# Performance work log

Hardware: AMD Instinct MI355X
Metric: run time of the kernel (lower is better)

The kernel has to match this reference:

```python
import jax, jax.numpy as jnp
import numpy as np


def setup_inputs() -> dict:
    key = jax.random.key(0)
    k1, k2, k3 = jax.random.split(key, 3)
    B, C, H, W = 4, 256, 96, 128
    F = 9
    return {
        "input1": jax.random.normal(k1, (B, C, H, W), dtype=jnp.float32),
        "input2": jax.random.normal(k2, (B, C, H, W), dtype=jnp.float32),
        "weights": jax.random.normal(k3, (C, F, F), dtype=jnp.float32),
        "filter_size": 9,
        "dilation": 2,
        "num_groups": 4,
    }


def _weighted_corr(input1, input2, weights, filter_size, dilation, num_groups):
    B, C, H, W = input1.shape
    F = filter_size
    G = num_groups
    Cg = C // G
    r = F // 2
    pad = r * dilation
    # zero-pad input2 spatially so out-of-bounds displacements contribute 0
    p2 = jnp.pad(input2, ((0, 0), (0, 0), (pad, pad), (pad, pad)))
    in1g = input1.reshape(B, G, Cg, H, W)
    outs = []  # one [B, G, H, W] map per window offset (dy, dx)
    for dy in range(F):
        for dx in range(F):
            shifted = p2[:, :, dy * dilation:dy * dilation + H,
                         dx * dilation:dx * dilation + W].reshape(B, G, Cg, H, W)
            wg = weights[:, dy, dx].reshape(G, Cg)
            outs.append(jnp.einsum('bgchw,bgchw,gc->bghw', in1g, shifted, wg))
    out = jnp.stack(outs, axis=2)  # [B, G, F*F, H, W]
    return out.reshape(B, G * F * F, H, W)


def reference(input1, input2, weights, filter_size, dilation, num_groups):
    return _weighted_corr(input1, input2, weights, filter_size, dilation, num_groups)
```

## Files before the change

### kernel.cpp

```cpp
#include <hip/hip_runtime.h>

#define B_   4
#define C_   256
#define H_   96
#define W_   128
#define F_   9
#define G_   4
#define CG   64
#define NC4  16
#define NO   81
#define TH   2
#define TCOLS (W_ + 16)
#define HW_  (H_ * W_)

#define NDY   3
#define PROWS (2 * NDY)
#define PTE   (PROWS * TCOLS)
#define PNK   4

typedef _Float16 half2v __attribute__((ext_vector_type(2)));
typedef unsigned u32x2 __attribute__((ext_vector_type(2)));

__device__ __forceinline__ half2v u2h(unsigned u) {
    half2v h; __builtin_memcpy(&h, &u, 4); return h;
}
__device__ __forceinline__ half2v pkrtz(float a, float b) {
    auto r = __builtin_amdgcn_cvt_pkrtz(a, b);
    half2v h; __builtin_memcpy(&h, &r, 4); return h;
}
__device__ __forceinline__ unsigned pkrtz_u(float a, float b) {
    auto r = __builtin_amdgcn_cvt_pkrtz(a, b);
    unsigned u; __builtin_memcpy(&u, &r, 4); return u;
}

#if __has_builtin(__builtin_amdgcn_fdot2)
#define FDOT2(a, b, c) __builtin_amdgcn_fdot2((a), (b), (c), false)
#else
__device__ __forceinline__ float fdot2_fb(half2v a, half2v b, float c) {
    return c + (float)a[0] * (float)b[0] + (float)a[1] * (float)b[1];
}
#define FDOT2(a, b, c) fdot2_fb((a), (b), (c))
#endif

__global__ void pack_weights_kernel(const float* __restrict__ w,
                                    u32x2* __restrict__ wp) {
    int i = blockIdx.x * blockDim.x + threadIdx.x;
    if (i >= G_ * NC4 * NO) return;
    int o  = i % NO;
    int c4 = (i / NO) % NC4;
    int g  = i / (NO * NC4);
    const float* base = w + (size_t)(g * CG + 4 * c4) * NO + o;
    u32x2 r;
    r.x = pkrtz_u(base[0], base[NO]);
    r.y = pkrtz_u(base[2 * NO], base[3 * NO]);
    wp[i] = r;
}

template <bool PACKED>
__global__ __launch_bounds__(256)
void wcorr_kernel(const float* __restrict__ in1, const float* __restrict__ in2,
                  const u32x2* __restrict__ wp, const float* __restrict__ wraw,
                  float* __restrict__ out) {
    __shared__ u32x2 tile[2][PTE];

    int bid  = blockIdx.x;
    int xcd  = bid & 7;
    int slot = bid >> 3;
    int pair = xcd + 8 * (slot / 144);
    int rem  = slot % 144;
    int pass = rem / 48;
    int hblk = rem % 48;
    int b = pair >> 2, g = pair & 3;
    int h0 = hblk * TH;

    int t  = threadIdx.x;
    int ty = t >> 7;
    int tx = t & 127;

    const float* in1g = in1 + (size_t)(b * C_ + g * CG) * HW_;
    const float* in2g = in2 + (size_t)(b * C_ + g * CG) * HW_;

    const int gr0 = h0 - 8 + 6 * pass;
    int po[PNK];
#pragma unroll
    for (int k = 0; k < PNK; ++k) {
        int idx = k * 256 + t;
        int row = idx / TCOLS;
        int col = idx - row * TCOLS;
        int gr  = gr0 + row;
        int gc  = col - 8;
        bool inb = (idx < PTE) && (gr >= 0) && (gr < H_) && (gc >= 0) && (gc < W_);
        po[k] = inb ? (gr * W_ + gc) : -1;
    }

    float acc[NDY * F_];
#pragma unroll
    for (int o = 0; o < NDY * F_; ++o) acc[o] = 0.f;

#pragma unroll
    for (int k = 0; k < PNK; ++k) {
        int idx = k * 256 + t;
        float v0 = 0.f, v1 = 0.f, v2 = 0.f, v3 = 0.f;
        if (po[k] >= 0) {
            const float* p = in2g + po[k];
            v0 = p[0]; v1 = p[HW_]; v2 = p[2 * HW_]; v3 = p[3 * HW_];
        }
        if (idx < PTE) {
            u32x2 r; r.x = pkrtz_u(v0, v1); r.y = pkrtz_u(v2, v3);
            tile[0][idx] = r;
        }
    }

    const int in1off = (h0 + ty) * W_ + tx;
    float a0 = in1g[in1off], a1 = in1g[in1off + HW_];
    float a2 = in1g[in1off + 2 * HW_], a3 = in1g[in1off + 3 * HW_];

    const int lbase = ty * TCOLS + tx;

    for (int c4 = 0; c4 < NC4; ++c4) {
        const bool more = (c4 + 1 < NC4);

        float v0[PNK], v1[PNK], v2[PNK], v3[PNK];
        if (more) {
            const float* chb = in2g + (size_t)(4 * (c4 + 1)) * HW_;
#pragma unroll
            for (int k = 0; k < PNK; ++k) {
                v0[k] = 0.f; v1[k] = 0.f; v2[k] = 0.f; v3[k] = 0.f;
                if (po[k] >= 0) {
                    const float* p = chb + po[k];
                    v0[k] = p[0]; v1[k] = p[HW_];
                    v2[k] = p[2 * HW_]; v3[k] = p[3 * HW_];
                }
            }
        }

        __syncthreads();

        if (more) {
            u32x2* dst = tile[(c4 + 1) & 1];
#pragma unroll
            for (int k = 0; k < PNK; ++k) {
                int idx = k * 256 + t;
                if (idx < PTE) {
                    u32x2 r; r.x = pkrtz_u(v0[k], v1[k]); r.y = pkrtz_u(v2[k], v3[k]);
                    dst[idx] = r;
                }
            }
        }

        const u32x2* lt = tile[c4 & 1];
        half2v ha = pkrtz(a0, a1);
        half2v hb = pkrtz(a2, a3);
        if (more) {
            const float* p = in1g + (size_t)(4 * (c4 + 1)) * HW_ + in1off;
            a0 = p[0]; a1 = p[HW_]; a2 = p[2 * HW_]; a3 = p[3 * HW_];
        }

        const u32x2* wrow = PACKED ? (wp + ((size_t)g * NC4 + c4) * NO + pass * NDY * F_) : nullptr;
        const float* wr = wraw + (size_t)(g * CG + 4 * c4) * NO + pass * NDY * F_;

#pragma unroll
        for (int dyp = 0; dyp < NDY; ++dyp) {
#pragma unroll
            for (int dx = 0; dx < F_; ++dx) {
                const int oo = dyp * F_ + dx;
                u32x2 uv = lt[lbase + dyp * 2 * TCOLS + dx * 2];
                half2v wa, wb;
                if (PACKED) {
                    u32x2 wv = wrow[oo];
                    wa = u2h(wv.x); wb = u2h(wv.y);
                } else {
                    wa = pkrtz(wr[oo], wr[oo + NO]);
                    wb = pkrtz(wr[oo + 2 * NO], wr[oo + 3 * NO]);
                }
                half2v p0 = wa * ha;
                half2v p1 = wb * hb;
                float s = FDOT2(p0, u2h(uv.x), acc[oo]);
                acc[oo]  = FDOT2(p1, u2h(uv.y), s);
            }
        }
    }

    size_t obase = (((size_t)pair * NO + pass * NDY * F_) * H_ + (h0 + ty)) * W_ + tx;
#pragma unroll
    for (int oo = 0; oo < NDY * F_; ++oo)
        out[obase + (size_t)oo * HW_] = acc[oo];
}

extern "C" void kernel_launch(void* const* d_in, const int* in_sizes, int n_in,
                              void* d_out, int out_size, void* d_ws, size_t ws_size,
                              hipStream_t stream) {
    const float* in1  = (const float*)d_in[0];
    const float* in2  = (const float*)d_in[1];
    const float* wraw = (const float*)d_in[2];
    float* out = (float*)d_out;

    const size_t wp_bytes = (size_t)G_ * NC4 * NO * 8;
    const int nblocks = 16 * 3 * (H_ / TH);

    if (ws_size >= wp_bytes) {
        u32x2* wp = (u32x2*)d_ws;
        int n = G_ * NC4 * NO;
        pack_weights_kernel<<<(n + 255) / 256, 256, 0, stream>>>(wraw, wp);
        wcorr_kernel<true><<<nblocks, 256, 0, stream>>>(in1, in2, wp, wraw, out);
    } else {
        wcorr_kernel<false><<<nblocks, 256, 0, stream>>>(in1, in2, nullptr, wraw, out);
    }
}
```

Measured before the change: 78.90 us.

## Split LDS tile by column parity and replace load branches with masks

The shared tile is reorganised so even and odd columns are stored in separate rows. A thread's nine dilated taps (stride 2) then become contiguous, and it can load all nine as a block per dy row, where before each tap was a separate strided access. Out-of-bounds global loads are now clamped to a valid address and zeroed with a packed half-precision mask multiply, which removes divergent branches from the staging loads. The cost is extra registers for the nine tap values and the mask, one extra packed multiply per staged element, and some redundant loads at the borders.

```diff
diff --git a/kernel.cpp b/kernel.cpp
--- a/kernel.cpp
+++ b/kernel.cpp
@@ -11,18 +11,23 @@
 #define NO   81
 #define TH   2
 #define TCOLS (W_ + 16)
+#define HCOL2 72
 #define HW_  (H_ * W_)
 
 #define NDY   3
 #define PROWS (2 * NDY)
 #define PTE   (PROWS * TCOLS)
 #define PNK   4
+#define TILE_E PTE
 
 typedef _Float16 half2v __attribute__((ext_vector_type(2)));
 typedef unsigned u32x2 __attribute__((ext_vector_type(2)));
 
 __device__ __forceinline__ half2v u2h(unsigned u) {
     half2v h; __builtin_memcpy(&h, &u, 4); return h;
+}
+__device__ __forceinline__ unsigned h2u(half2v h) {
+    unsigned u; __builtin_memcpy(&u, &h, 4); return u;
 }
 __device__ __forceinline__ half2v pkrtz(float a, float b) {
     auto r = __builtin_amdgcn_cvt_pkrtz(a, b);
@@ -61,7 +66,7 @@
 void wcorr_kernel(const float* __restrict__ in1, const float* __restrict__ in2,
                   const u32x2* __restrict__ wp, const float* __restrict__ wraw,
                   float* __restrict__ out) {
-    __shared__ u32x2 tile[2][PTE];
+    __shared__ u32x2 tile[2][TILE_E];
 
     int bid  = blockIdx.x;
     int xcd  = bid & 7;
@@ -82,32 +87,39 @@
 
     const int gr0 = h0 - 8 + 6 * pass;
     int po[PNK];
+    unsigned msk[PNK];
+    int lix[PNK];
 #pragma unroll
     for (int k = 0; k < PNK; ++k) {
-        int idx = k * 256 + t;
-        int row = idx / TCOLS;
-        int col = idx - row * TCOLS;
-        int gr  = gr0 + row;
-        int gc  = col - 8;
-        bool inb = (idx < PTE) && (gr >= 0) && (gr < H_) && (gc >= 0) && (gc < W_);
-        po[k] = inb ? (gr * W_ + gc) : -1;
+        int pidx = k * 256 + t;
+        int row  = pidx / TCOLS;
+        int hcol = pidx - row * TCOLS;
+        int gr = gr0 + row, gc = hcol - 8;
+        bool inb = (pidx < PTE) && gr >= 0 && gr < H_ && gc >= 0 && gc < W_;
+        int off = gr * W_ + gc;
+        off = off < 0 ? 0 : (off > HW_ - 1 ? HW_ - 1 : off);
+        po[k]  = off;
+        float m = inb ? 1.f : 0.f;
+        msk[k] = pkrtz_u(m, m);
+        lix[k] = (row * 2 + (hcol & 1)) * HCOL2 + (hcol >> 1);
     }
 
     float acc[NDY * F_];
 #pragma unroll
     for (int o = 0; o < NDY * F_; ++o) acc[o] = 0.f;
 
-#pragma unroll
-    for (int k = 0; k < PNK; ++k) {
-        int idx = k * 256 + t;
-        float v0 = 0.f, v1 = 0.f, v2 = 0.f, v3 = 0.f;
-        if (po[k] >= 0) {
-            const float* p = in2g + po[k];
-            v0 = p[0]; v1 = p[HW_]; v2 = p[2 * HW_]; v3 = p[3 * HW_];
-        }
-        if (idx < PTE) {
-            u32x2 r; r.x = pkrtz_u(v0, v1); r.y = pkrtz_u(v2, v3);
-            tile[0][idx] = r;
+    {
+#pragma unroll
+        for (int k = 0; k < PNK; ++k) {
+            float v0 = in2g[po[k]],           v1 = in2g[po[k] + HW_];
+            float v2 = in2g[po[k] + 2 * HW_], v3 = in2g[po[k] + 3 * HW_];
+            if (k < PNK - 1 || t < PTE - (PNK - 1) * 256) {
+                half2v m = u2h(msk[k]);
+                u32x2 r;
+                r.x = h2u(u2h(pkrtz_u(v0, v1)) * m);
+                r.y = h2u(u2h(pkrtz_u(v2, v3)) * m);
+                tile[0][lix[k]] = r;
+            }
         }
     }
 
@@ -115,7 +127,8 @@
     float a0 = in1g[in1off], a1 = in1g[in1off + HW_];
     float a2 = in1g[in1off + 2 * HW_], a3 = in1g[in1off + 3 * HW_];
 
-    const int lbase = ty * TCOLS + tx;
+    const int p     = tx & 1;
+    const int cbase = tx >> 1;
 
     for (int c4 = 0; c4 < NC4; ++c4) {
         const bool more = (c4 + 1 < NC4);
@@ -125,12 +138,8 @@
             const float* chb = in2g + (size_t)(4 * (c4 + 1)) * HW_;
 #pragma unroll
             for (int k = 0; k < PNK; ++k) {
-                v0[k] = 0.f; v1[k] = 0.f; v2[k] = 0.f; v3[k] = 0.f;
-                if (po[k] >= 0) {
-                    const float* p = chb + po[k];
-                    v0[k] = p[0]; v1[k] = p[HW_];
-                    v2[k] = p[2 * HW_]; v3[k] = p[3 * HW_];
-                }
+                v0[k] = chb[po[k]];           v1[k] = chb[po[k] + HW_];
+                v2[k] = chb[po[k] + 2 * HW_]; v3[k] = chb[po[k] + 3 * HW_];
             }
         }
 
@@ -140,10 +149,12 @@
             u32x2* dst = tile[(c4 + 1) & 1];
 #pragma unroll
             for (int k = 0; k < PNK; ++k) {
-                int idx = k * 256 + t;
-                if (idx < PTE) {
-                    u32x2 r; r.x = pkrtz_u(v0[k], v1[k]); r.y = pkrtz_u(v2[k], v3[k]);
-                    dst[idx] = r;
+                if (k < PNK - 1 || t < PTE - (PNK - 1) * 256) {
+                    half2v m = u2h(msk[k]);
+                    u32x2 r;
+                    r.x = h2u(u2h(pkrtz_u(v0[k], v1[k])) * m);
+                    r.y = h2u(u2h(pkrtz_u(v2[k], v3[k])) * m);
+                    dst[lix[k]] = r;
                 }
             }
         }
@@ -152,8 +163,8 @@
         half2v ha = pkrtz(a0, a1);
         half2v hb = pkrtz(a2, a3);
         if (more) {
-            const float* p = in1g + (size_t)(4 * (c4 + 1)) * HW_ + in1off;
-            a0 = p[0]; a1 = p[HW_]; a2 = p[2 * HW_]; a3 = p[3 * HW_];
+            const float* pp = in1g + (size_t)(4 * (c4 + 1)) * HW_ + in1off;
+            a0 = pp[0]; a1 = pp[HW_]; a2 = pp[2 * HW_]; a3 = pp[3 * HW_];
         }
 
         const u32x2* wrow = PACKED ? (wp + ((size_t)g * NC4 + c4) * NO + pass * NDY * F_) : nullptr;
@@ -161,10 +172,14 @@
 
 #pragma unroll
         for (int dyp = 0; dyp < NDY; ++dyp) {
+            const u32x2* eb = lt + ((2 * dyp + ty) * 2 + p) * HCOL2 + cbase;
+            u32x2 e[9];
+#pragma unroll
+            for (int k = 0; k < 9; ++k) e[k] = eb[k];
+
 #pragma unroll
             for (int dx = 0; dx < F_; ++dx) {
                 const int oo = dyp * F_ + dx;
-                u32x2 uv = lt[lbase + dyp * 2 * TCOLS + dx * 2];
                 half2v wa, wb;
                 if (PACKED) {
                     u32x2 wv = wrow[oo];
@@ -175,8 +190,8 @@
                 }
                 half2v p0 = wa * ha;
                 half2v p1 = wb * hb;
-                float s = FDOT2(p0, u2h(uv.x), acc[oo]);
-                acc[oo]  = FDOT2(p1, u2h(uv.y), s);
+                float s = FDOT2(p0, u2h(e[dx].x), acc[oo]);
+                acc[oo]  = FDOT2(p1, u2h(e[dx].y), s);
             }
         }
     }
```

Result: slower. 80.53 us (+2.1%).
